# Performance work log

Measured on AMD Instinct MI355X. Metric: run time of the kernel, lower is better.

Reference implementation:

```python
import jax, jax.numpy as jnp
import numpy as np

B, S, E, H = 8, 2048, 512, 8
D = E // H  # head_dim = 64


def setup_inputs() -> dict:
    key0 = jax.random.key(0)
    ks = jax.random.split(key0, 12)
    scale = 1.0 / np.sqrt(E)
    return {
        "value": jax.random.normal(ks[0], (B, S, E), jnp.float32),
        "key": jax.random.normal(ks[1], (B, S, E), jnp.float32),
        "query": jax.random.normal(ks[2], (B, S, E), jnp.float32),
        "mask": jax.random.randint(ks[3], (B, 1, 1, S), 0, 2, jnp.int32),
        "wq": jax.random.normal(ks[4], (E, E), jnp.float32) * scale,
        "bq": jnp.zeros((E,), jnp.float32),
        "wk": jax.random.normal(ks[5], (E, E), jnp.float32) * scale,
        "bk": jnp.zeros((E,), jnp.float32),
        "wv": jax.random.normal(ks[6], (E, E), jnp.float32) * scale,
        "bv": jnp.zeros((E,), jnp.float32),
        "wo": jax.random.normal(ks[7], (E, E), jnp.float32) * scale,
        "bo": jnp.zeros((E,), jnp.float32),
    }


def reference(value, key, query, mask, wq, bq, wk, bk, wv, bv, wo, bo):
    b, s, e = query.shape
    # projections
    q = (query @ wq + bq).reshape(b, s, H, D)  # (B,S,H,D)
    k = (key @ wk + bk).reshape(b, s, H, D)
    v = (value @ wv + bv).reshape(b, s, H, D)
    # scaled dot-product logits: (B,H,Sq,Sk)
    logits = jnp.einsum("bqhd,bkhd->bhqk", q, k) / jnp.sqrt(jnp.asarray(D, q.dtype))
    logits = logits + mask.astype(logits.dtype) * -1e9  # mask==1 -> blocked
    attn = jax.nn.softmax(logits, axis=-1)
    out = jnp.einsum("bhqk,bkhd->bqhd", attn, v).reshape(b, s, e)
    return out @ wo + bo
```

## Files before the change

kernel.cpp:

```cpp
#include <hip/hip_runtime.h>

#define Bz 8
#define Sz 2048
#define Ez 512
#define Hz 8
#define Dz 64

typedef _Float16 f16;
typedef __attribute__((ext_vector_type(2))) _Float16 f16x2;
typedef __attribute__((ext_vector_type(8))) _Float16 f16x8;
typedef __attribute__((ext_vector_type(4))) float f32x4;

#define LOG2E 1.44269504f

__device__ __forceinline__ void async16(const void* g, void* l) {
    __builtin_amdgcn_global_load_lds(
        (const __attribute__((address_space(1))) unsigned int*)g,
        (__attribute__((address_space(3))) unsigned int*)l, 16, 0, 0);
}

__device__ __forceinline__ f16x2 pkrtz(float a, float b) {
    return __builtin_bit_cast(f16x2, __builtin_amdgcn_cvt_pkrtz(a, b));
}

__device__ __forceinline__ int swz(int row) {
    return (row & 7) ^ ((2 * ((row >> 3) & 3)) & 7);
}

__global__ __launch_bounds__(256)
void cast_kernel(const float* __restrict__ q, const float* __restrict__ k,
                 const float* __restrict__ v,
                 f16* __restrict__ qa, f16* __restrict__ ka, f16* __restrict__ va)
{
    const int z = blockIdx.y;
    const int idx = blockIdx.x * 256 + threadIdx.x;
    const float* src = (z == 0) ? q : (z == 1) ? k : v;
    f16* dst = (z == 0) ? qa : (z == 1) ? ka : va;
    float4 x = *(const float4*)&src[(size_t)idx * 4];
    f16x2 h0 = pkrtz(x.x, x.y), h1 = pkrtz(x.z, x.w);
    f16 h[4] = {h0[0], h0[1], h1[0], h1[1]};
    *(uint2*)&dst[(size_t)idx * 4] = *(uint2*)h;
}

__global__ __launch_bounds__(256)
void prep_w(const float* __restrict__ W0, const float* __restrict__ W1,
            const float* __restrict__ W2, const float* __restrict__ W3,
            f16* __restrict__ T0, f16* __restrict__ T1,
            f16* __restrict__ T2, f16* __restrict__ T3)
{
    __shared__ float S[64][68];
    const float* W = (blockIdx.z==0)?W0:(blockIdx.z==1)?W1:(blockIdx.z==2)?W2:W3;
    f16*         T = (blockIdx.z==0)?T0:(blockIdx.z==1)?T1:(blockIdx.z==2)?T2:T3;
    const float sc = (blockIdx.z == 0) ? 0.125f * LOG2E : 1.0f;
    const int k0 = blockIdx.x * 64, n0 = blockIdx.y * 64;
    const int tid = threadIdx.x;
    {
        int kr = tid >> 4, nc = (tid & 15) * 4;
        #pragma unroll
        for (int i = 0; i < 4; ++i) {
            float4 w4 = *(const float4*)&W[(size_t)(k0 + kr + i*16) * Ez + n0 + nc];
            S[kr + i*16][nc+0] = w4.x; S[kr + i*16][nc+1] = w4.y;
            S[kr + i*16][nc+2] = w4.z; S[kr + i*16][nc+3] = w4.w;
        }
    }
    __syncthreads();
    {
        int n = tid >> 2, kq = tid & 3;
        f16 h[16];
        #pragma unroll
        for (int j = 0; j < 16; ++j) h[j] = (f16)(S[kq*16 + j][n] * sc);
        f16* dst = &T[(size_t)(n0 + n) * Ez + k0 + kq*16];
        *(uint4*)&dst[0] = *(uint4*)&h[0];
        *(uint4*)&dst[8] = *(uint4*)&h[8];
    }
}

__global__ __launch_bounds__(256)
void mask_index(const int* __restrict__ mask, int* __restrict__ idx,
                int* __restrict__ slen)
{
    __shared__ int sc2[2][256];
    __shared__ int stot;
    const int b = blockIdx.x, tid = threadIdx.x;
    const int* mp = mask + (size_t)b * Sz;
    int m[8], c = 0;
    #pragma unroll
    for (int j = 0; j < 8; ++j) { m[j] = mp[tid*8 + j]; c += (m[j] == 0); }
    sc2[0][tid] = c;
    __syncthreads();
    int src = 0;
    #pragma unroll
    for (int s = 1; s < 256; s <<= 1) {
        int v = sc2[src][tid] + ((tid >= s) ? sc2[src][tid - s] : 0);
        sc2[src ^ 1][tid] = v;
        src ^= 1;
        __syncthreads();
    }
    int incl = sc2[src][tid];
    int base = incl - c;
    if (tid == 255) { slen[b] = incl; stot = incl; }
    int k = base;
    #pragma unroll
    for (int j = 0; j < 8; ++j)
        if (m[j] == 0) idx[(size_t)b * Sz + (k++)] = tid*8 + j;
    __syncthreads();
    for (int j = stot + tid; j < Sz; j += 256) idx[(size_t)b * Sz + j] = 0;
}

__global__ __launch_bounds__(256)
void compact_v(const f16* __restrict__ vp, const int* __restrict__ idx,
               const int* __restrict__ slen, f16* __restrict__ vt)
{
    const int ct = blockIdx.x, h = blockIdx.y, b = blockIdx.z;
    const int sl = slen[b];
    if (ct * 64 >= sl) {
        if (ct > 0 || sl > 0) return;
    }
    __shared__ f16 S[64 * 72];
    const int tid = threadIdx.x;
    {
        int r = tid >> 2, ch = tid & 3;
        int j = ct * 64 + r;
        uint4 v0 = {0,0,0,0}, v1 = {0,0,0,0};
        if (j < sl) {
            int s = idx[(size_t)b * Sz + j];
            const f16* srcp = vp + (((size_t)b * Hz + h) * Sz + s) * Dz + ch * 16;
            v0 = *(const uint4*)&srcp[0];
            v1 = *(const uint4*)&srcp[8];
        }
        *(uint4*)&S[r*72 + ch*16]     = v0;
        *(uint4*)&S[r*72 + ch*16 + 8] = v1;
    }
    __syncthreads();
    {
        int d = tid >> 2, kq = tid & 3;
        f16 hh[16];
        #pragma unroll
        for (int j = 0; j < 16; ++j) hh[j] = S[(kq*16 + j)*72 + d];
        f16* dst = vt + (((size_t)b * Hz + h) * Dz + d) * Sz + ct*64 + kq*16;
        *(uint4*)&dst[0] = *(uint4*)&hh[0];
        *(uint4*)&dst[8] = *(uint4*)&hh[8];
    }
}

__global__ __launch_bounds__(256, 4)
void proj_gemm(const f16* __restrict__ qa, const f16* __restrict__ ka,
               const f16* __restrict__ va,
               const f16* __restrict__ wtq, const f16* __restrict__ wtk,
               const f16* __restrict__ wtv,
               const float* __restrict__ bqp, const float* __restrict__ bkp,
               const float* __restrict__ bvp,
               f16* __restrict__ qp, f16* __restrict__ kp, f16* __restrict__ vp)
{
    __shared__ __align__(16) char lds[18432];
    const int z = blockIdx.z;
    const f16* A  = (z==0)?qa:(z==1)?ka:va;
    const f16* Wt = (z==0)?wtq:(z==1)?wtk:wtv;
    const float* bias = (z==0)?bqp:(z==1)?bkp:bvp;
    f16* C16 = (z==0)?qp:(z==1)?kp:vp;
    const float bscale = (z==0) ? 0.125f*LOG2E : 1.0f;

    const int tid  = threadIdx.x;
    const int lane = tid & 63, w = tid >> 6;
    const int col  = lane & 15, quad = lane >> 4;
    const int wm = w & 1, wn = w >> 1;
    const int m0 = blockIdx.x * 128, n0 = blockIdx.y * 128;
    const int srow = lane >> 2, schunk = lane & 3;

    f16* As = (f16*)lds;
    f16* Ws = As + 4096;

    f32x4 acc[4][4];
    #pragma unroll
    for (int i = 0; i < 4; ++i)
        #pragma unroll
        for (int j = 0; j < 4; ++j) acc[i][j] = (f32x4){0.f,0.f,0.f,0.f};

    const int xrc = (col >> 1) & 3;

    for (int t = 0; t < 16; ++t) {
        __syncthreads();
        #pragma unroll
        for (int i = 0; i < 2; ++i) {
            int row = w*32 + i*16 + srow;
            int cl = schunk ^ ((row >> 1) & 3);
            async16(&A[(size_t)(m0 + row) * Ez + t*32 + cl*8],  &As[row*32 + schunk*8]);
            async16(&Wt[(size_t)(n0 + row) * Ez + t*32 + cl*8], &Ws[row*32 + schunk*8]);
        }
        __syncthreads();
        f16x8 af[4];
        #pragma unroll
        for (int mi = 0; mi < 4; ++mi)
            af[mi] = *(const f16x8*)&As[(wm*64 + mi*16 + col)*32 + ((quad ^ xrc)*8)];
        #pragma unroll
        for (int ni = 0; ni < 4; ++ni) {
            f16x8 wf = *(const f16x8*)&Ws[(wn*64 + ni*16 + col)*32 + ((quad ^ xrc)*8)];
            #pragma unroll
            for (int mi = 0; mi < 4; ++mi)
                acc[mi][ni] = __builtin_amdgcn_mfma_f32_16x16x32_f16(af[mi], wf, acc[mi][ni], 0,0,0);
        }
    }

    f16* Tr = (f16*)lds;
    #pragma unroll
    for (int p = 0; p < 2; ++p) {
        __syncthreads();
        if (wn == p) {
            #pragma unroll
            for (int ni = 0; ni < 4; ++ni) {
                float bv = bias[n0 + p*64 + ni*16 + col] * bscale;
                #pragma unroll
                for (int mi = 0; mi < 4; ++mi)
                    #pragma unroll
                    for (int rr = 0; rr < 4; ++rr) {
                        int ml = wm*64 + mi*16 + quad*4 + rr;
                        Tr[ml*72 + ni*16 + col] = (f16)(acc[mi][ni][rr] + bv);
                    }
            }
        }
        __syncthreads();
        int rw = tid >> 1, half = tid & 1;
        int m = m0 + rw, b = m >> 11, s = m & (Sz-1);
        int hh = (n0 >> 6) + p;
        f16* dst = &C16[(((size_t)b*Hz + hh)*Sz + s)*Dz + half*32];
        const f16* srcp = &Tr[rw*72 + half*32];
        #pragma unroll
        for (int j = 0; j < 4; ++j)
            *(uint4*)&dst[j*8] = *(const uint4*)&srcp[j*8];
    }
}

__global__ __launch_bounds__(256, 4)
void out_gemm(const f16* __restrict__ A, const f16* __restrict__ Wt,
              const float* __restrict__ bias, float* __restrict__ Cf)
{
    __shared__ __align__(16) char lds[16384];
    const int tid  = threadIdx.x;
    const int lane = tid & 63, w = tid >> 6;
    const int col  = lane & 15, quad = lane >> 4;
    const int wm = w & 1, wn = w >> 1;
    const int m0 = blockIdx.x * 128, n0 = blockIdx.y * 128;
    const int srow = lane >> 2, schunk = lane & 3;

    f16* As = (f16*)lds;
    f16* Ws = As + 4096;

    f32x4 acc[4][4];
    #pragma unroll
    for (int i = 0; i < 4; ++i)
        #pragma unroll
        for (int j = 0; j < 4; ++j) acc[i][j] = (f32x4){0.f,0.f,0.f,0.f};

    const int xrc = (col >> 1) & 3;

    for (int t = 0; t < 16; ++t) {
        __syncthreads();
        #pragma unroll
        for (int i = 0; i < 2; ++i) {
            int row = w*32 + i*16 + srow;
            int cl = schunk ^ ((row >> 1) & 3);
            async16(&A[(size_t)(m0 + row) * Ez + t*32 + cl*8],  &As[row*32 + schunk*8]);
            async16(&Wt[(size_t)(n0 + row) * Ez + t*32 + cl*8], &Ws[row*32 + schunk*8]);
        }
        __syncthreads();
        f16x8 af[4];
        #pragma unroll
        for (int mi = 0; mi < 4; ++mi)
            af[mi] = *(const f16x8*)&As[(wm*64 + mi*16 + col)*32 + ((quad ^ xrc)*8)];
        #pragma unroll
        for (int ni = 0; ni < 4; ++ni) {
            f16x8 wf = *(const f16x8*)&Ws[(wn*64 + ni*16 + col)*32 + ((quad ^ xrc)*8)];
            #pragma unroll
            for (int mi = 0; mi < 4; ++mi)
                acc[mi][ni] = __builtin_amdgcn_mfma_f32_16x16x32_f16(af[mi], wf, acc[mi][ni], 0,0,0);
        }
    }

    #pragma unroll
    for (int ni = 0; ni < 4; ++ni) {
        int n = n0 + wn*64 + ni*16 + col;
        float bv = bias[n];
        #pragma unroll
        for (int mi = 0; mi < 4; ++mi)
            #pragma unroll
            for (int rr = 0; rr < 4; ++rr) {
                int m = m0 + wm*64 + mi*16 + quad*4 + rr;
                Cf[(size_t)m * Ez + n] = acc[mi][ni][rr] + bv;
            }
    }
}

__global__ __launch_bounds__(256, 4)
void attn_f16(const f16* __restrict__ Q, const f16* __restrict__ K,
              const f16* __restrict__ VT, const int* __restrict__ idx,
              const int* __restrict__ slen, f16* __restrict__ O)
{
    __shared__ __align__(16) f16 KS[2][64*64];
    __shared__ __align__(16) f16 VS[2][64*64];

    const int tid  = threadIdx.x;
    const int lane = tid & 63, w = tid >> 6;
    const int col  = lane & 15, quad = lane >> 4;

    const int blk = blockIdx.x;
    const int xcd = blk & 7, slot = blk >> 3;
    const int bh = xcd + 8 * (slot >> 4);
    const int qb = slot & 15;
    const int b = bh >> 3, h = bh & 7;

    const int sl = slen[b];
    const int nt = (sl + 63) >> 6;

    const int q0 = qb * 128 + w * 32;

    f16x8 qf[2][2];
    #pragma unroll
    for (int qt = 0; qt < 2; ++qt)
        #pragma unroll
        for (int ks = 0; ks < 2; ++ks)
            qf[qt][ks] = *(const f16x8*)&Q[((size_t)bh*Sz + q0 + qt*16 + col)*Dz + ks*32 + quad*8];

    const f16* Kp = K + (size_t)bh * Sz * Dz;
    const f16* Vp = VT + (size_t)bh * Dz * Sz;
    const int* ixp = idx + (size_t)b * Sz;

    const int srow = lane >> 3, sch = lane & 7;
    const int row0 = w*16 + srow, row1 = row0 + 8;
    const int g0 = swz(row0), g1 = swz(row1);
    const int cl0 = sch ^ g0, cl1 = sch ^ g1;

    int keyrow[4], gk[4];
    #pragma unroll
    for (int kc = 0; kc < 4; ++kc) {
        keyrow[kc] = 32*(kc>>1) + 8*(col>>2) + 4*(kc&1) + (col&3);
        gk[kc] = swz(keyrow[kc]);
    }

    f32x4 oacc[2][4];
    #pragma unroll
    for (int qt = 0; qt < 2; ++qt)
        #pragma unroll
        for (int dc = 0; dc < 4; ++dc) oacc[qt][dc] = (f32x4){0.f,0.f,0.f,0.f};
    float lsum[2] = {0.f, 0.f};

    auto issue = [&](int t, int buf, int s0, int s1) {
        async16(&Kp[(size_t)s0*Dz + cl0*8],          &KS[buf][row0*64 + sch*8]);
        async16(&Vp[(size_t)row0*Sz + t*64 + cl0*8], &VS[buf][row0*64 + sch*8]);
        async16(&Kp[(size_t)s1*Dz + cl1*8],          &KS[buf][row1*64 + sch*8]);
        async16(&Vp[(size_t)row1*Sz + t*64 + cl1*8], &VS[buf][row1*64 + sch*8]);
    };

    int cs0 = ixp[row0], cs1 = ixp[row1];
    issue(0, 0, cs0, cs1);
    int ns0 = 0, ns1 = 0;
    if (nt > 1) { ns0 = ixp[64 + row0]; ns1 = ixp[64 + row1]; }

    for (int t = 0; t < nt; ++t) {
        const int cur = t & 1;
        __syncthreads();
        if (t + 1 < nt) {
            issue(t + 1, cur ^ 1, ns0, ns1);
            if (t + 2 < nt) {
                ns0 = ixp[(t+2)*64 + row0];
                ns1 = ixp[(t+2)*64 + row1];
            }
        }

        f32x4 sc[2][4];
        #pragma unroll
        for (int qt = 0; qt < 2; ++qt)
            #pragma unroll
            for (int kc = 0; kc < 4; ++kc) sc[qt][kc] = (f32x4){0.f,0.f,0.f,0.f};
        #pragma unroll
        for (int kc = 0; kc < 4; ++kc) {
            #pragma unroll
            for (int ks = 0; ks < 2; ++ks) {
                f16x8 kf = *(const f16x8*)&KS[cur][keyrow[kc]*64 + (((ks*4 + quad) ^ gk[kc])*8)];
                sc[0][kc] = __builtin_amdgcn_mfma_f32_16x16x32_f16(kf, qf[0][ks], sc[0][kc], 0,0,0);
                sc[1][kc] = __builtin_amdgcn_mfma_f32_16x16x32_f16(kf, qf[1][ks], sc[1][kc], 0,0,0);
            }
        }

        const bool last = (t == nt - 1);
        union { f16x2 h2[4]; f16x8 h8; } ph[2][2];
        #pragma unroll
        for (int qt = 0; qt < 2; ++qt) {
            #pragma unroll
            for (int kg = 0; kg < 2; ++kg) {
                float e0 = exp2f(sc[qt][2*kg][0]), e1 = exp2f(sc[qt][2*kg][1]);
                float e2 = exp2f(sc[qt][2*kg][2]), e3 = exp2f(sc[qt][2*kg][3]);
                float e4 = exp2f(sc[qt][2*kg+1][0]), e5 = exp2f(sc[qt][2*kg+1][1]);
                float e6 = exp2f(sc[qt][2*kg+1][2]), e7 = exp2f(sc[qt][2*kg+1][3]);
                float ls;
                if (last) {
                    int rem = sl - t*64 - 32*kg - 8*quad;
                    ls = ((rem > 0 ? e0 : 0.f) + (rem > 1 ? e1 : 0.f))
                       + ((rem > 2 ? e2 : 0.f) + (rem > 3 ? e3 : 0.f))
                       + ((rem > 4 ? e4 : 0.f) + (rem > 5 ? e5 : 0.f))
                       + ((rem > 6 ? e6 : 0.f) + (rem > 7 ? e7 : 0.f));
                } else {
                    ls = ((e0 + e1) + (e2 + e3)) + ((e4 + e5) + (e6 + e7));
                }
                lsum[qt] += ls;
                ph[qt][kg].h2[0] = pkrtz(e0, e1);
                ph[qt][kg].h2[1] = pkrtz(e2, e3);
                ph[qt][kg].h2[2] = pkrtz(e4, e5);
                ph[qt][kg].h2[3] = pkrtz(e6, e7);
            }
        }

        #pragma unroll
        for (int dc = 0; dc < 4; ++dc) {
            const int d = dc*16 + col;
            const int gd = swz(d);
            #pragma unroll
            for (int kg = 0; kg < 2; ++kg) {
                f16x8 vf = *(const f16x8*)&VS[cur][d*64 + (((kg*4 + quad) ^ gd)*8)];
                oacc[0][dc] = __builtin_amdgcn_mfma_f32_16x16x32_f16(vf, ph[0][kg].h8, oacc[0][dc], 0,0,0);
                oacc[1][dc] = __builtin_amdgcn_mfma_f32_16x16x32_f16(vf, ph[1][kg].h8, oacc[1][dc], 0,0,0);
            }
        }
    }

    float inv[2];
    #pragma unroll
    for (int qt = 0; qt < 2; ++qt) {
        float v = lsum[qt];
        v += __shfl_xor(v, 16, 64);
        v += __shfl_xor(v, 32, 64);
        inv[qt] = 1.0f / v;
    }
    #pragma unroll
    for (int qt = 0; qt < 2; ++qt) {
        const int q = q0 + qt*16 + col;
        f16* op = &O[((size_t)b*Sz + q)*Ez + h*Dz];
        #pragma unroll
        for (int dc = 0; dc < 4; ++dc) {
            f16 ov[4] = {(f16)(oacc[qt][dc][0]*inv[qt]), (f16)(oacc[qt][dc][1]*inv[qt]),
                         (f16)(oacc[qt][dc][2]*inv[qt]), (f16)(oacc[qt][dc][3]*inv[qt])};
            *(uint2*)&op[dc*16 + quad*4] = *(uint2*)ov;
        }
    }
}

extern "C" void kernel_launch(void* const* d_in, const int* in_sizes, int n_in,
                              void* d_out, int out_size, void* d_ws, size_t ws_size,
                              hipStream_t stream)
{
    const float* value = (const float*)d_in[0];
    const float* key   = (const float*)d_in[1];
    const float* query = (const float*)d_in[2];
    const int*   mask  = (const int*)d_in[3];
    const float* wq = (const float*)d_in[4];
    const float* bq = (const float*)d_in[5];
    const float* wk = (const float*)d_in[6];
    const float* bk = (const float*)d_in[7];
    const float* wv = (const float*)d_in[8];
    const float* bv = (const float*)d_in[9];
    const float* wo = (const float*)d_in[10];
    const float* bo = (const float*)d_in[11];
    float* out = (float*)d_out;

    const size_t nW   = (size_t)Ez * Ez;
    const size_t nAct = (size_t)Bz * Sz * Ez;
    f16* wtq = (f16*)d_ws;
    f16* wtk = wtq + nW;
    f16* wtv = wtk + nW;
    f16* wto = wtv + nW;
    f16* qa  = wto + nW;
    f16* ka  = qa + nAct;
    f16* va  = ka + nAct;
    f16* qp  = va + nAct;
    f16* kp  = qp + nAct;
    f16* vp  = kp + nAct;
    f16* vt  = vp + nAct;
    f16* o16 = vt + nAct;
    int* idxp = (int*)(o16 + nAct);
    int* slenp = idxp + Bz * Sz;

    cast_kernel<<<dim3(8192, 3), 256, 0, stream>>>(query, key, value, qa, ka, va);
    prep_w<<<dim3(8, 8, 4), 256, 0, stream>>>(wq, wk, wv, wo, wtq, wtk, wtv, wto);
    mask_index<<<Bz, 256, 0, stream>>>(mask, idxp, slenp);

    proj_gemm<<<dim3(128, 4, 3), 256, 0, stream>>>(qa, ka, va, wtq, wtk, wtv,
                                                   bq, bk, bv, qp, kp, vp);

    compact_v<<<dim3(32, Hz, Bz), 256, 0, stream>>>(vp, idxp, slenp, vt);

    attn_f16<<<1024, 256, 0, stream>>>(qp, kp, vt, idxp, slenp, o16);

    out_gemm<<<dim3(128, 4), 256, 0, stream>>>(o16, wto, bo, out);
}
```

Before: 300.5 us.

## Compute softmax row sums via MFMA with ones row in V and retile out_gemm

Appends extra rows to the transposed V buffer (VTR=80): row 64 holds 1.0 for valid compacted keys and the rest are zero, so one extra MFMA per key group produces the softmax denominator. This replaces the per-lane scalar exp sums, the tail masking on the last tile, and the cross-lane shuffle reduction. The out-projection GEMM also switches to 128x64 tiles so it launches twice as many blocks. The cost is extra V traffic and LDS per tile and a larger workspace.

```diff
diff --git a/kernel.cpp b/kernel.cpp
--- a/kernel.cpp
+++ b/kernel.cpp
@@ -5,6 +5,7 @@
 #define Ez 512
 #define Hz 8
 #define Dz 64
+#define VTR 80
 
 typedef _Float16 f16;
 typedef __attribute__((ext_vector_type(2))) _Float16 f16x2;
@@ -113,9 +114,7 @@
 {
     const int ct = blockIdx.x, h = blockIdx.y, b = blockIdx.z;
     const int sl = slen[b];
-    if (ct * 64 >= sl) {
-        if (ct > 0 || sl > 0) return;
-    }
+    if (ct * 64 >= sl && !(ct == 0 && sl == 0)) return;
     __shared__ f16 S[64 * 72];
     const int tid = threadIdx.x;
     {
@@ -132,14 +131,24 @@
         *(uint4*)&S[r*72 + ch*16 + 8] = v1;
     }
     __syncthreads();
+    f16* base = vt + ((size_t)b * Hz + h) * VTR * Sz;
     {
         int d = tid >> 2, kq = tid & 3;
         f16 hh[16];
         #pragma unroll
         for (int j = 0; j < 16; ++j) hh[j] = S[(kq*16 + j)*72 + d];
-        f16* dst = vt + (((size_t)b * Hz + h) * Dz + d) * Sz + ct*64 + kq*16;
+        f16* dst = base + (size_t)d * Sz + ct*64 + kq*16;
         *(uint4*)&dst[0] = *(uint4*)&hh[0];
         *(uint4*)&dst[8] = *(uint4*)&hh[8];
+    }
+    if (tid < 128) {
+        int row = 64 + (tid >> 3);
+        int c0 = (tid & 7) * 8;
+        f16 hh[8];
+        #pragma unroll
+        for (int j = 0; j < 8; ++j)
+            hh[j] = (row == 64 && (ct*64 + c0 + j) < sl) ? (f16)1.0f : (f16)0.0f;
+        *(uint4*)&base[(size_t)row * Sz + ct*64 + c0] = *(uint4*)hh;
     }
 }
 
@@ -234,20 +243,18 @@
 void out_gemm(const f16* __restrict__ A, const f16* __restrict__ Wt,
               const float* __restrict__ bias, float* __restrict__ Cf)
 {
-    __shared__ __align__(16) char lds[16384];
+    __shared__ __align__(16) f16 smem[6144];
+    f16* As = smem;
+    f16* Ws = smem + 4096;
+
     const int tid  = threadIdx.x;
     const int lane = tid & 63, w = tid >> 6;
     const int col  = lane & 15, quad = lane >> 4;
-    const int wm = w & 1, wn = w >> 1;
-    const int m0 = blockIdx.x * 128, n0 = blockIdx.y * 128;
-    const int srow = lane >> 2, schunk = lane & 3;
-
-    f16* As = (f16*)lds;
-    f16* Ws = As + 4096;
-
-    f32x4 acc[4][4];
-    #pragma unroll
-    for (int i = 0; i < 4; ++i)
+    const int m0 = blockIdx.x * 128, n0 = blockIdx.y * 64;
+
+    f32x4 acc[2][4];
+    #pragma unroll
+    for (int i = 0; i < 2; ++i)
         #pragma unroll
         for (int j = 0; j < 4; ++j) acc[i][j] = (f32x4){0.f,0.f,0.f,0.f};
 
@@ -257,34 +264,40 @@
         __syncthreads();
         #pragma unroll
         for (int i = 0; i < 2; ++i) {
-            int row = w*32 + i*16 + srow;
-            int cl = schunk ^ ((row >> 1) & 3);
-            async16(&A[(size_t)(m0 + row) * Ez + t*32 + cl*8],  &As[row*32 + schunk*8]);
-            async16(&Wt[(size_t)(n0 + row) * Ez + t*32 + cl*8], &Ws[row*32 + schunk*8]);
-        }
-        __syncthreads();
-        f16x8 af[4];
-        #pragma unroll
-        for (int mi = 0; mi < 4; ++mi)
-            af[mi] = *(const f16x8*)&As[(wm*64 + mi*16 + col)*32 + ((quad ^ xrc)*8)];
+            int row = i*64 + (tid >> 2);
+            int ch = tid & 3;
+            int cl = ch ^ ((row >> 1) & 3);
+            async16(&A[(size_t)(m0 + row) * Ez + t*32 + cl*8], &As[row*32 + ch*8]);
+        }
+        {
+            int row = tid >> 2;
+            int ch = tid & 3;
+            int cl = ch ^ ((row >> 1) & 3);
+            async16(&Wt[(size_t)(n0 + row) * Ez + t*32 + cl*8], &Ws[row*32 + ch*8]);
+        }
+        __syncthreads();
+        f16x8 af[2];
+        #pragma unroll
+        for (int mi = 0; mi < 2; ++mi)
+            af[mi] = *(const f16x8*)&As[(w*32 + mi*16 + col)*32 + ((quad ^ xrc)*8)];
         #pragma unroll
         for (int ni = 0; ni < 4; ++ni) {
-            f16x8 wf = *(const f16x8*)&Ws[(wn*64 + ni*16 + col)*32 + ((quad ^ xrc)*8)];
-            #pragma unroll
-            for (int mi = 0; mi < 4; ++mi)
+            f16x8 wf = *(const f16x8*)&Ws[(ni*16 + col)*32 + ((quad ^ xrc)*8)];
+            #pragma unroll
+            for (int mi = 0; mi < 2; ++mi)
                 acc[mi][ni] = __builtin_amdgcn_mfma_f32_16x16x32_f16(af[mi], wf, acc[mi][ni], 0,0,0);
         }
     }
 
     #pragma unroll
     for (int ni = 0; ni < 4; ++ni) {
-        int n = n0 + wn*64 + ni*16 + col;
+        int n = n0 + ni*16 + col;
         float bv = bias[n];
         #pragma unroll
-        for (int mi = 0; mi < 4; ++mi)
+        for (int mi = 0; mi < 2; ++mi)
             #pragma unroll
             for (int rr = 0; rr < 4; ++rr) {
-                int m = m0 + wm*64 + mi*16 + quad*4 + rr;
+                int m = m0 + w*32 + mi*16 + quad*4 + rr;
                 Cf[(size_t)m * Ez + n] = acc[mi][ni][rr] + bv;
             }
     }
@@ -296,7 +309,7 @@
               const int* __restrict__ slen, f16* __restrict__ O)
 {
     __shared__ __align__(16) f16 KS[2][64*64];
-    __shared__ __align__(16) f16 VS[2][64*64];
+    __shared__ __align__(16) f16 VS[2][VTR*64];
 
     const int tid  = threadIdx.x;
     const int lane = tid & 63, w = tid >> 6;
@@ -309,7 +322,8 @@
     const int b = bh >> 3, h = bh & 7;
 
     const int sl = slen[b];
-    const int nt = (sl + 63) >> 6;
+    int nt = (sl + 63) >> 6;
+    if (nt < 1) nt = 1;
 
     const int q0 = qb * 128 + w * 32;
 
@@ -321,13 +335,14 @@
             qf[qt][ks] = *(const f16x8*)&Q[((size_t)bh*Sz + q0 + qt*16 + col)*Dz + ks*32 + quad*8];
 
     const f16* Kp = K + (size_t)bh * Sz * Dz;
-    const f16* Vp = VT + (size_t)bh * Dz * Sz;
+    const f16* Vp = VT + (size_t)bh * VTR * Sz;
     const int* ixp = idx + (size_t)b * Sz;
 
     const int srow = lane >> 3, sch = lane & 7;
     const int row0 = w*16 + srow, row1 = row0 + 8;
-    const int g0 = swz(row0), g1 = swz(row1);
-    const int cl0 = sch ^ g0, cl1 = sch ^ g1;
+    const int cl0 = sch ^ swz(row0), cl1 = sch ^ swz(row1);
+    const int rowe = 64 + 8*w + srow;
+    const int cle = sch ^ swz(rowe);
 
     int keyrow[4], gk[4];
     #pragma unroll
@@ -335,19 +350,23 @@
         keyrow[kc] = 32*(kc>>1) + 8*(col>>2) + 4*(kc&1) + (col&3);
         gk[kc] = swz(keyrow[kc]);
     }
+    const int rowo = 64 + col;
+    const int go = swz(rowo);
 
     f32x4 oacc[2][4];
     #pragma unroll
     for (int qt = 0; qt < 2; ++qt)
         #pragma unroll
         for (int dc = 0; dc < 4; ++dc) oacc[qt][dc] = (f32x4){0.f,0.f,0.f,0.f};
-    float lsum[2] = {0.f, 0.f};
+    f32x4 lsacc[2] = {(f32x4){0.f,0.f,0.f,0.f}, (f32x4){0.f,0.f,0.f,0.f}};
 
     auto issue = [&](int t, int buf, int s0, int s1) {
         async16(&Kp[(size_t)s0*Dz + cl0*8],          &KS[buf][row0*64 + sch*8]);
         async16(&Vp[(size_t)row0*Sz + t*64 + cl0*8], &VS[buf][row0*64 + sch*8]);
         async16(&Kp[(size_t)s1*Dz + cl1*8],          &KS[buf][row1*64 + sch*8]);
         async16(&Vp[(size_t)row1*Sz + t*64 + cl1*8], &VS[buf][row1*64 + sch*8]);
+        if (w < 2)
+            async16(&Vp[(size_t)rowe*Sz + t*64 + cle*8], &VS[buf][rowe*64 + sch*8]);
     };
 
     int cs0 = ixp[row0], cs1 = ixp[row1];
@@ -381,7 +400,6 @@
             }
         }
 
-        const bool last = (t == nt - 1);
         union { f16x2 h2[4]; f16x8 h8; } ph[2][2];
         #pragma unroll
         for (int qt = 0; qt < 2; ++qt) {
@@ -391,17 +409,6 @@
                 float e2 = exp2f(sc[qt][2*kg][2]), e3 = exp2f(sc[qt][2*kg][3]);
                 float e4 = exp2f(sc[qt][2*kg+1][0]), e5 = exp2f(sc[qt][2*kg+1][1]);
                 float e6 = exp2f(sc[qt][2*kg+1][2]), e7 = exp2f(sc[qt][2*kg+1][3]);
-                float ls;
-                if (last) {
-                    int rem = sl - t*64 - 32*kg - 8*quad;
-                    ls = ((rem > 0 ? e0 : 0.f) + (rem > 1 ? e1 : 0.f))
-                       + ((rem > 2 ? e2 : 0.f) + (rem > 3 ? e3 : 0.f))
-                       + ((rem > 4 ? e4 : 0.f) + (rem > 5 ? e5 : 0.f))
-                       + ((rem > 6 ? e6 : 0.f) + (rem > 7 ? e7 : 0.f));
-                } else {
-                    ls = ((e0 + e1) + (e2 + e3)) + ((e4 + e5) + (e6 + e7));
-                }
-                lsum[qt] += ls;
                 ph[qt][kg].h2[0] = pkrtz(e0, e1);
                 ph[qt][kg].h2[1] = pkrtz(e2, e3);
                 ph[qt][kg].h2[2] = pkrtz(e4, e5);
@@ -410,6 +417,13 @@
         }
 
         #pragma unroll
+        for (int kg = 0; kg < 2; ++kg) {
+            f16x8 of = *(const f16x8*)&VS[cur][rowo*64 + (((kg*4 + quad) ^ go)*8)];
+            lsacc[0] = __builtin_amdgcn_mfma_f32_16x16x32_f16(of, ph[0][kg].h8, lsacc[0], 0,0,0);
+            lsacc[1] = __builtin_amdgcn_mfma_f32_16x16x32_f16(of, ph[1][kg].h8, lsacc[1], 0,0,0);
+        }
+
+        #pragma unroll
         for (int dc = 0; dc < 4; ++dc) {
             const int d = dc*16 + col;
             const int gd = swz(d);
@@ -425,10 +439,8 @@
     float inv[2];
     #pragma unroll
     for (int qt = 0; qt < 2; ++qt) {
-        float v = lsum[qt];
-        v += __shfl_xor(v, 16, 64);
-        v += __shfl_xor(v, 32, 64);
-        inv[qt] = 1.0f / v;
+        float lv = __shfl(lsacc[qt][0], col, 64);
+        inv[qt] = 1.0f / lv;
     }
     #pragma unroll
     for (int qt = 0; qt < 2; ++qt) {
@@ -463,6 +475,7 @@
 
     const size_t nW   = (size_t)Ez * Ez;
     const size_t nAct = (size_t)Bz * Sz * Ez;
+    const size_t nVT  = (size_t)Bz * Hz * VTR * Sz;
     f16* wtq = (f16*)d_ws;
     f16* wtk = wtq + nW;
     f16* wtv = wtk + nW;
@@ -474,7 +487,7 @@
     f16* kp  = qp + nAct;
     f16* vp  = kp + nAct;
     f16* vt  = vp + nAct;
-    f16* o16 = vt + nAct;
+    f16* o16 = vt + nVT;
     int* idxp = (int*)(o16 + nAct);
     int* slenp = idxp + Bz * Sz;
 
@@ -489,5 +502,5 @@
 
     attn_f16<<<1024, 256, 0, stream>>>(qp, kp, vt, idxp, slenp, o16);
 
-    out_gemm<<<dim3(128, 4), 256, 0, stream>>>(o16, wto, bo, out);
-}
+    out_gemm<<<dim3(128, 8), 256, 0, stream>>>(o16, wto, bo, out);
+}
```

New measurement: 301.1 us. No clear change (+0.2%).
